# Performance work log

Hardware: AMD Instinct MI355X
Metric: run time of the kernel (lower is better)

The kernel has to match this reference:

```python
import jax, jax.numpy as jnp
import numpy as np
from jax import lax

A = 9            # 3 scales * 3 ratios
H, W = 100, 100  # feature map
STRIDE = 16
PRE_NMS = 6000
POST_NMS = 300
NMS_THRESH = 0.7


def _make_anchors():
    """Standard py-faster-rcnn anchor grid, index order (h, w, a)."""
    base_size = 16.0
    ratios = np.array([0.5, 1.0, 2.0])
    scales = np.array([8.0, 16.0, 32.0])
    x_ctr = y_ctr = (base_size - 1.0) / 2.0
    size = base_size * base_size
    ws_r = np.round(np.sqrt(size / ratios))            # [3]
    hs_r = np.round(ws_r * ratios)                     # [3]
    ws = (ws_r[:, None] * scales[None, :]).reshape(-1)  # [9]
    hs = (hs_r[:, None] * scales[None, :]).reshape(-1)  # [9]
    base = np.stack([x_ctr - 0.5 * (ws - 1), y_ctr - 0.5 * (hs - 1),
                     x_ctr + 0.5 * (ws - 1), y_ctr + 0.5 * (hs - 1)], axis=1)  # [9,4]
    sx, sy = np.meshgrid(np.arange(W) * STRIDE, np.arange(H) * STRIDE)
    shifts = np.stack([sx.ravel(), sy.ravel(), sx.ravel(), sy.ravel()], axis=1)  # [H*W,4]
    anchors = (shifts[:, None, :] + base[None, :, :]).reshape(-1, 4)             # [H*W*A,4]
    return anchors.astype(np.float32)


def setup_inputs() -> dict:
    key = jax.random.key(0)
    k1, k2, k3 = jax.random.split(key, 3)
    return {
        "anchors": jnp.asarray(_make_anchors()),
        "rpn_cls_prob": jax.random.uniform(k1, (1, H, W, 2 * A), dtype=jnp.float32),
        "rpn_bbox_pred": jax.random.normal(k2, (1, H, W, 4 * A), dtype=jnp.float32) * 0.1,
        "rpn_trans_param": jax.random.normal(k3, (1, H, W, 6 * A), dtype=jnp.float32) * 0.1,
        "im_info": jnp.array([H * STRIDE, W * STRIDE, 1.0], dtype=jnp.float32),
    }


def _bbox_transform_inv(anchors, deltas):
    w = anchors[:, 2] - anchors[:, 0] + 1.0
    h = anchors[:, 3] - anchors[:, 1] + 1.0
    cx = anchors[:, 0] + 0.5 * w
    cy = anchors[:, 1] + 0.5 * h
    dx, dy, dw, dh = deltas[:, 0], deltas[:, 1], deltas[:, 2], deltas[:, 3]
    pcx = dx * w + cx
    pcy = dy * h + cy
    pw = jnp.exp(dw) * w
    ph = jnp.exp(dh) * h
    return jnp.stack([pcx - 0.5 * pw, pcy - 0.5 * ph,
                      pcx + 0.5 * pw, pcy + 0.5 * ph], axis=1)


def _clip_boxes(boxes, im_hw):
    im_h, im_w = im_hw[0], im_hw[1]
    x1 = jnp.clip(boxes[:, 0], 0.0, im_w - 1.0)
    y1 = jnp.clip(boxes[:, 1], 0.0, im_h - 1.0)
    x2 = jnp.clip(boxes[:, 2], 0.0, im_w - 1.0)
    y2 = jnp.clip(boxes[:, 3], 0.0, im_h - 1.0)
    return jnp.stack([x1, y1, x2, y2], axis=1)


def _nms_mask(boxes, thresh):
    """Greedy NMS on score-sorted boxes; returns keep mask [N] bool."""
    n = boxes.shape[0]
    x1, y1, x2, y2 = boxes[:, 0], boxes[:, 1], boxes[:, 2], boxes[:, 3]
    areas = (x2 - x1 + 1.0) * (y2 - y1 + 1.0)
    idx = jnp.arange(n)

    def body(i, keep):
        xx1 = jnp.maximum(x1[i], x1)
        yy1 = jnp.maximum(y1[i], y1)
        xx2 = jnp.minimum(x2[i], x2)
        yy2 = jnp.minimum(y2[i], y2)
        iw = jnp.maximum(xx2 - xx1 + 1.0, 0.0)
        ih = jnp.maximum(yy2 - yy1 + 1.0, 0.0)
        inter = iw * ih
        iou = inter / (areas[i] + areas - inter)
        suppress = (iou > thresh) & (idx > i) & keep[i]
        return keep & (~suppress)

    return lax.fori_loop(0, n, body, jnp.ones((n,), dtype=bool))


def _forward(anchors, rpn_cls_prob, rpn_bbox_pred, rpn_trans_param, im_info):
    scores = rpn_cls_prob[:, :, :, A:].reshape(-1)      # fg probs, order (h,w,a)
    deltas = rpn_bbox_pred.reshape(-1, 4)
    trans = rpn_trans_param.reshape(-1, 6)

    proposals = _bbox_transform_inv(anchors, deltas)
    proposals = _clip_boxes(proposals, im_info[:2])

    order = jnp.argsort(-scores)[:PRE_NMS]
    scores = scores[order]
    proposals = proposals[order]
    trans = trans[order]

    keep = _nms_mask(proposals, NMS_THRESH)
    # fixed-size keep indices (score-descending order preserved); padded with 0
    keep_idx = jnp.where(keep, size=POST_NMS, fill_value=0)[0]

    proposals = proposals[keep_idx]
    scores = scores[keep_idx]
    trans = trans[keep_idx]

    batch_inds = jnp.zeros((proposals.shape[0], 1), dtype=proposals.dtype)
    blob = jnp.concatenate([batch_inds, proposals], axis=1)  # [POST_NMS, 5]
    return blob, scores, trans


def reference(anchors, rpn_cls_prob, rpn_bbox_pred, rpn_trans_param, im_info):
    return _forward(anchors, rpn_cls_prob, rpn_bbox_pred, rpn_trans_param, im_info)
```

## Files before the change

kernel.cpp:

```cpp
#include <hip/hip_runtime.h>
#include <stdint.h>
#include <math.h>

#define A_ 9
#define N_ANCH 90000
#define PRE_NMS 6000
#define POST_NMS 300
#define NMS_TH 0.7f
#define NBINS 4096
#define SLOT_CAP 64
#define RANK_BINS 512
#define MASK_W 94
#define NTILE 4465

#define OFF_BCNT   0u
#define OFF_BUCKET 16384u
#define OFF_ORDER  2113536u
#define OFF_TSCORE 2137536u
#define OFF_TBOX   2161536u
#define OFF_MASK   2257536u

typedef unsigned long long u64;
typedef unsigned int u32;

__device__ __forceinline__ int score_bin(float s) {
    int bin = (int)(s * (float)NBINS);
    return bin < 0 ? 0 : (bin > NBINS - 1 ? NBINS - 1 : bin);
}

__global__ void __launch_bounds__(256) k_zero(int4* __restrict__ bcnt4) {
#pragma unroll
    for (int k = 0; k < 4; ++k)
        bcnt4[k * 256 + threadIdx.x] = make_int4(0, 0, 0, 0);
}

__global__ void k_scatter(const float* __restrict__ cls,
                          int* __restrict__ bucketCnt,
                          u64* __restrict__ buckets) {
    int n = blockIdx.x * blockDim.x + threadIdx.x;
    if (n >= N_ANCH) return;
    float s = cls[(n / A_) * (2 * A_) + A_ + (n % A_)];
    int bin = score_bin(s);
    int slot = atomicAdd(&bucketCnt[bin], 1);
    if (slot < SLOT_CAP) {
        u64 key = ((u64)__float_as_uint(s) << 32) | (u64)(0xFFFFFFFFu - (u32)n);
        buckets[(size_t)bin * SLOT_CAP + slot] = key;
    }
}

__device__ __forceinline__ int block_scan(const int* __restrict__ hist,
                                          int* sufs, int* sfx, int* tsh,
                                          int hl[16]) {
    int t = threadIdx.x;
    int csum = 0;
#pragma unroll
    for (int k = 0; k < 16; ++k) { hl[k] = hist[t * 16 + k]; csum += hl[k]; }
    sfx[t] = csum;
    if (t == 0) *tsh = 0;
    __syncthreads();
    for (int off = 1; off < 256; off <<= 1) {
        int v = (t + off < 256) ? sfx[t + off] : 0;
        __syncthreads();
        sfx[t] += v;
        __syncthreads();
    }
    int acc = sfx[t] - csum;
    int best = -1;
#pragma unroll
    for (int k = 15; k >= 0; --k) {
        sufs[t * 16 + k] = acc;
        acc += hl[k];
        if (best < 0 && acc >= PRE_NMS) best = t * 16 + k;
    }
    if (best >= 0) atomicMax(tsh, best);
    __syncthreads();
    return *tsh;
}

__global__ void __launch_bounds__(256) k_rank(const u64* __restrict__ buckets,
                                              const int* __restrict__ bucketCnt,
                                              const float* __restrict__ anchors,
                                              const float* __restrict__ bbox,
                                              const float* __restrict__ im_info,
                                              int* __restrict__ order,
                                              float* __restrict__ tscore,
                                              float* __restrict__ tb) {
#pragma clang fp contract(off)
    __shared__ int sufs[NBINS];
    __shared__ int sfx[256];
    __shared__ int tsh;
    int hl[16];
    int T = block_scan(bucketCnt, sufs, sfx, &tsh, hl);
    int gid = blockIdx.x * 256 + threadIdx.x;
    int bin = (NBINS - RANK_BINS) + (gid >> 6);
    int slot = gid & (SLOT_CAP - 1);
    if (bin < T) return;
    int cnt = bucketCnt[bin];
    if (cnt > SLOT_CAP) cnt = SLOT_CAP;
    if (slot >= cnt) return;
    const u64* bk = buckets + (size_t)bin * SLOT_CAP;
    u64 ki = bk[slot];
    int rank = sufs[bin];
    for (int j = 0; j < cnt; ++j)
        rank += (bk[j] > ki) ? 1 : 0;
    if (rank >= PRE_NMS) return;

    int n = (int)(0xFFFFFFFFu - (u32)(ki & 0xFFFFFFFFull));
    order[rank] = n;
    tscore[rank] = __uint_as_float((u32)(ki >> 32));

    int hw = n / A_, a = n % A_;
    const float* an = anchors + (size_t)n * 4;
    const float* d  = bbox + (size_t)hw * (4 * A_) + a * 4;
    float w  = an[2] - an[0] + 1.0f;
    float h  = an[3] - an[1] + 1.0f;
    float cx = an[0] + 0.5f * w;
    float cy = an[1] + 0.5f * h;
    float pcx = d[0] * w + cx;
    float pcy = d[1] * h + cy;
    float pw  = expf(d[2]) * w;
    float ph  = expf(d[3]) * h;
    float x1 = pcx - 0.5f * pw;
    float y1 = pcy - 0.5f * ph;
    float x2 = pcx + 0.5f * pw;
    float y2 = pcy + 0.5f * ph;
    float im_h = im_info[0], im_w = im_info[1];
    x1 = fminf(fmaxf(x1, 0.0f), im_w - 1.0f);
    y1 = fminf(fmaxf(y1, 0.0f), im_h - 1.0f);
    x2 = fminf(fmaxf(x2, 0.0f), im_w - 1.0f);
    y2 = fminf(fmaxf(y2, 0.0f), im_h - 1.0f);
    tb[rank * 4 + 0] = x1;
    tb[rank * 4 + 1] = y1;
    tb[rank * 4 + 2] = x2;
    tb[rank * 4 + 3] = y2;
}

__global__ void __launch_bounds__(64) k_mask(const float* __restrict__ tb,
                                             u64* __restrict__ mask) {
#pragma clang fp contract(off)
    int u = NTILE - 1 - (int)blockIdx.x;
    int k = (int)((sqrtf(8.0f * (float)u + 1.0f) - 1.0f) * 0.5f);
    while ((k + 1) * (k + 2) / 2 <= u) ++k;
    while (k > 0 && k * (k + 1) / 2 > u) --k;
    int jdx = u - k * (k + 1) / 2;
    int rb = 93 - k, cb = 93 - jdx;

    __shared__ float cbx[64][4];
    __shared__ float car[64];
    int t = threadIdx.x;
    int j0 = cb * 64;
    int jj = j0 + t;
    if (jj < PRE_NMS) {
        float bx1 = tb[jj * 4 + 0], by1 = tb[jj * 4 + 1];
        float bx2 = tb[jj * 4 + 2], by2 = tb[jj * 4 + 3];
        cbx[t][0] = bx1; cbx[t][1] = by1; cbx[t][2] = bx2; cbx[t][3] = by2;
        car[t] = (bx2 - bx1 + 1.0f) * (by2 - by1 + 1.0f);
    } else {
        cbx[t][0] = 0; cbx[t][1] = 0; cbx[t][2] = -2; cbx[t][3] = -2;
        car[t] = 1.0f;
    }
    __syncthreads();
    int row = rb * 64 + t;
    if (row >= PRE_NMS) return;
    float x1 = tb[row * 4 + 0], y1 = tb[row * 4 + 1];
    float x2 = tb[row * 4 + 2], y2 = tb[row * 4 + 3];
    float ai = (x2 - x1 + 1.0f) * (y2 - y1 + 1.0f);
    u64 bits = 0;
    for (int c = 0; c < 64; ++c) {
        int j = j0 + c;
        if (j > row && j < PRE_NMS) {
            float xx1 = fmaxf(x1, cbx[c][0]);
            float yy1 = fmaxf(y1, cbx[c][1]);
            float xx2 = fminf(x2, cbx[c][2]);
            float yy2 = fminf(y2, cbx[c][3]);
            float iw = fmaxf(xx2 - xx1 + 1.0f, 0.0f);
            float ih = fmaxf(yy2 - yy1 + 1.0f, 0.0f);
            float inter = iw * ih;
            float iou = inter / (ai + car[c] - inter);
            if (iou > NMS_TH) bits |= (1ull << c);
        }
    }
    mask[(size_t)row * MASK_W + cb] = bits;
}

__global__ void __launch_bounds__(256) k_reduce_out(const u64* __restrict__ mask,
                                                    const int* __restrict__ order,
                                                    const float* __restrict__ tb,
                                                    const float* __restrict__ tscore,
                                                    const float* __restrict__ trans,
                                                    float* __restrict__ out) {
    __shared__ int keep_s[POST_NMS];
    if (threadIdx.x < 64) {
        const int lane = threadIdx.x;
        int cnt = 0;
        u64 cur = 0;
        u64 dwc = mask[(size_t)lane * MASK_W + 0];
        for (int c = 0; c < MASK_W; ++c) {
            int nc = c + 1;
            u64 dwn = 0;
            if (nc < MASK_W) {
                int rn = nc * 64 + lane;
                if (rn < PRE_NMS) dwn = mask[(size_t)rn * MASK_W + nc];
            }
            int nrows = PRE_NMS - c * 64; if (nrows > 64) nrows = 64;
            u64 vm = (nrows >= 64) ? ~0ull : ((1ull << nrows) - 1ull);
            u32 dlo_v = (u32)dwc, dhi_v = (u32)(dwc >> 32);
            int cnt0 = cnt;
            u64 keptw = 0;
            u64 freeb = (~cur) & vm;
            while (freeb != 0ull && cnt < POST_NMS) {
                u32 bs;
                asm("s_ff1_i32_b64 %0, %1" : "=s"(bs) : "s"(freeb));
                u32 dlo, dhi;
                asm("v_readlane_b32 %0, %1, %2" : "=s"(dlo) : "v"(dlo_v), "s"(bs));
                asm("v_readlane_b32 %0, %1, %2" : "=s"(dhi) : "v"(dhi_v), "s"(bs));
                u64 bit = 1ull << bs;
                keptw |= bit;
                cur |= (((u64)dhi << 32) | (u64)dlo) | bit;
                cnt++;
                freeb = (~cur) & vm;
            }
            if ((keptw >> lane) & 1ull) {
                int pos = cnt0 + __popcll(keptw & ((1ull << lane) - 1ull));
                keep_s[pos] = c * 64 + lane;
            }
            if (cnt >= POST_NMS || nc >= MASK_W) break;
            u64 acc = 0;
#pragma unroll
            for (int s = 0; s < 5; ++s) {
                int p = s * 64 + lane;
                if (p < cnt) {
                    int kr = keep_s[p];
                    acc |= mask[(size_t)kr * MASK_W + nc];
                }
            }
#pragma unroll
            for (int m = 32; m >= 1; m >>= 1)
                acc |= (u64)__shfl_xor((unsigned long long)acc, m, 64);
            u32 clo = __builtin_amdgcn_readfirstlane((u32)acc);
            u32 chi = __builtin_amdgcn_readfirstlane((u32)(acc >> 32));
            cur = ((u64)chi << 32) | (u64)clo;
            dwc = dwn;
        }
        for (int r = cnt + lane; r < POST_NMS; r += 64) keep_s[r] = 0;
    }
    __syncthreads();
    for (int row = threadIdx.x; row < POST_NMS; row += 256) {
        int r = keep_s[row];
        int n = order[r];
        out[row * 5 + 0] = 0.0f;
        out[row * 5 + 1] = tb[r * 4 + 0];
        out[row * 5 + 2] = tb[r * 4 + 1];
        out[row * 5 + 3] = tb[r * 4 + 2];
        out[row * 5 + 4] = tb[r * 4 + 3];
        out[POST_NMS * 5 + row] = tscore[r];
        int hw = n / A_, a = n % A_;
        const float* tp = trans + (size_t)hw * (6 * A_) + a * 6;
#pragma unroll
        for (int c = 0; c < 6; ++c)
            out[POST_NMS * 6 + row * 6 + c] = tp[c];
    }
}

extern "C" void kernel_launch(void* const* d_in, const int* in_sizes, int n_in,
                              void* d_out, int out_size, void* d_ws, size_t ws_size,
                              hipStream_t stream) {
    const float* anchors = (const float*)d_in[0];
    const float* cls     = (const float*)d_in[1];
    const float* bbox    = (const float*)d_in[2];
    const float* trans   = (const float*)d_in[3];
    const float* im_info = (const float*)d_in[4];
    float* out = (float*)d_out;
    char* ws = (char*)d_ws;

    int*   bcnt    = (int*)(ws + OFF_BCNT);
    u64*   buckets = (u64*)(ws + OFF_BUCKET);
    int*   order   = (int*)(ws + OFF_ORDER);
    float* tscore  = (float*)(ws + OFF_TSCORE);
    float* tb      = (float*)(ws + OFF_TBOX);
    u64*   mask    = (u64*)(ws + OFF_MASK);

    int nb = (N_ANCH + 255) / 256;
    k_zero<<<1, 256, 0, stream>>>((int4*)bcnt);
    k_scatter<<<nb, 256, 0, stream>>>(cls, bcnt, buckets);
    k_rank<<<(RANK_BINS * SLOT_CAP) / 256, 256, 0, stream>>>(buckets, bcnt,
                                                             anchors, bbox, im_info,
                                                             order, tscore, tb);
    k_mask<<<NTILE, 64, 0, stream>>>(tb, mask);
    k_reduce_out<<<1, 256, 0, stream>>>(mask, order, tb, tscore, trans, out);
}
```

Measured before the change: 73.92 us.

## Replace full NMS mask kernel with lazy single-block NMS over kept boxes

Drops the precomputed 6000x6000 IoU bitmask kernel and its reduction kernel. In their place is one single-block kernel that stages the top 2048 boxes in LDS, precomputes diagonal 64x64 chunk masks, and for each next chunk tests candidates only against boxes already kept. Because NMS stops once 300 boxes are kept, only a few chunks are likely to be processed, which avoids the O(N^2) mask work and a kernel launch. The cost is serialized per-chunk work on a single CU with two barriers per chunk, and fallback global loads for rows past 2048.

```diff
diff --git a/kernel.cpp b/kernel.cpp
--- a/kernel.cpp
+++ b/kernel.cpp
@@ -11,14 +11,14 @@
 #define SLOT_CAP 64
 #define RANK_BINS 512
 #define MASK_W 94
-#define NTILE 4465
+#define LDSROWS 2048
+#define CPRE 16
 
 #define OFF_BCNT   0u
 #define OFF_BUCKET 16384u
 #define OFF_ORDER  2113536u
 #define OFF_TSCORE 2137536u
 #define OFF_TBOX   2161536u
-#define OFF_MASK   2257536u
 
 typedef unsigned long long u64;
 typedef unsigned int u32;
@@ -135,73 +135,56 @@
     tb[rank * 4 + 3] = y2;
 }
 
-__global__ void __launch_bounds__(64) k_mask(const float* __restrict__ tb,
-                                             u64* __restrict__ mask) {
+__device__ __forceinline__ bool iou_gt(float4 rb, float ra, float4 cb, float ca) {
 #pragma clang fp contract(off)
-    int u = NTILE - 1 - (int)blockIdx.x;
-    int k = (int)((sqrtf(8.0f * (float)u + 1.0f) - 1.0f) * 0.5f);
-    while ((k + 1) * (k + 2) / 2 <= u) ++k;
-    while (k > 0 && k * (k + 1) / 2 > u) --k;
-    int jdx = u - k * (k + 1) / 2;
-    int rb = 93 - k, cb = 93 - jdx;
-
-    __shared__ float cbx[64][4];
-    __shared__ float car[64];
-    int t = threadIdx.x;
-    int j0 = cb * 64;
-    int jj = j0 + t;
-    if (jj < PRE_NMS) {
-        float bx1 = tb[jj * 4 + 0], by1 = tb[jj * 4 + 1];
-        float bx2 = tb[jj * 4 + 2], by2 = tb[jj * 4 + 3];
-        cbx[t][0] = bx1; cbx[t][1] = by1; cbx[t][2] = bx2; cbx[t][3] = by2;
-        car[t] = (bx2 - bx1 + 1.0f) * (by2 - by1 + 1.0f);
-    } else {
-        cbx[t][0] = 0; cbx[t][1] = 0; cbx[t][2] = -2; cbx[t][3] = -2;
-        car[t] = 1.0f;
-    }
-    __syncthreads();
-    int row = rb * 64 + t;
-    if (row >= PRE_NMS) return;
-    float x1 = tb[row * 4 + 0], y1 = tb[row * 4 + 1];
-    float x2 = tb[row * 4 + 2], y2 = tb[row * 4 + 3];
-    float ai = (x2 - x1 + 1.0f) * (y2 - y1 + 1.0f);
-    u64 bits = 0;
-    for (int c = 0; c < 64; ++c) {
-        int j = j0 + c;
-        if (j > row && j < PRE_NMS) {
-            float xx1 = fmaxf(x1, cbx[c][0]);
-            float yy1 = fmaxf(y1, cbx[c][1]);
-            float xx2 = fminf(x2, cbx[c][2]);
-            float yy2 = fminf(y2, cbx[c][3]);
-            float iw = fmaxf(xx2 - xx1 + 1.0f, 0.0f);
-            float ih = fmaxf(yy2 - yy1 + 1.0f, 0.0f);
-            float inter = iw * ih;
-            float iou = inter / (ai + car[c] - inter);
-            if (iou > NMS_TH) bits |= (1ull << c);
-        }
-    }
-    mask[(size_t)row * MASK_W + cb] = bits;
-}
-
-__global__ void __launch_bounds__(256) k_reduce_out(const u64* __restrict__ mask,
-                                                    const int* __restrict__ order,
-                                                    const float* __restrict__ tb,
-                                                    const float* __restrict__ tscore,
-                                                    const float* __restrict__ trans,
-                                                    float* __restrict__ out) {
-    __shared__ int keep_s[POST_NMS];
-    if (threadIdx.x < 64) {
-        const int lane = threadIdx.x;
-        int cnt = 0;
-        u64 cur = 0;
-        u64 dwc = mask[(size_t)lane * MASK_W + 0];
-        for (int c = 0; c < MASK_W; ++c) {
-            int nc = c + 1;
-            u64 dwn = 0;
-            if (nc < MASK_W) {
-                int rn = nc * 64 + lane;
-                if (rn < PRE_NMS) dwn = mask[(size_t)rn * MASK_W + nc];
-            }
+    float xx1 = fmaxf(rb.x, cb.x);
+    float yy1 = fmaxf(rb.y, cb.y);
+    float xx2 = fminf(rb.z, cb.z);
+    float yy2 = fminf(rb.w, cb.w);
+    float iw = fmaxf(xx2 - xx1 + 1.0f, 0.0f);
+    float ih = fmaxf(yy2 - yy1 + 1.0f, 0.0f);
+    float inter = iw * ih;
+    return inter / (ra + ca - inter) > NMS_TH;
+}
+
+__global__ void __launch_bounds__(256)
+k_nms(const float4* __restrict__ tb4, const int* __restrict__ order,
+      const float* __restrict__ tscore, const float* __restrict__ trans,
+      float* __restrict__ out) {
+#pragma clang fp contract(off)
+    __shared__ float4 sbox[LDSROWS];
+    __shared__ float  sarea[LDSROWS];
+    __shared__ u64    sdiag[CPRE][64];
+    __shared__ int    keep_s[POST_NMS];
+    __shared__ u64    curq[4];
+    __shared__ int    ctrl[2];
+    const int t = threadIdx.x;
+    const int lane = t & 63, wq = t >> 6;
+
+    for (int i = t; i < LDSROWS; i += 256) {
+        float4 b = tb4[i];
+        sbox[i] = b;
+        sarea[i] = (b.z - b.x + 1.0f) * (b.w - b.y + 1.0f);
+    }
+    if (t == 0) { ctrl[0] = 0; ctrl[1] = 0; }
+    __syncthreads();
+    for (int g = t; g < CPRE * 64; g += 256) {
+        int ch = g >> 6, row = g & 63;
+        float4 rb = sbox[g]; float ra = sarea[g];
+        u64 bits = 0;
+        for (int c = row + 1; c < 64; ++c) {
+            int j = ch * 64 + c;
+            if (iou_gt(rb, ra, sbox[j], sarea[j])) bits |= 1ull << c;
+        }
+        sdiag[ch][row] = bits;
+    }
+    __syncthreads();
+
+    int cnt = 0;
+    u64 cur = 0;
+    for (int c = 0; c < MASK_W; ++c) {
+        if (wq == 0) {
+            u64 dwc = sdiag[c & (CPRE - 1)][lane];
             int nrows = PRE_NMS - c * 64; if (nrows > 64) nrows = 64;
             u64 vm = (nrows >= 64) ? ~0ull : ((1ull << nrows) - 1ull);
             u32 dlo_v = (u32)dwc, dhi_v = (u32)(dwc >> 32);
@@ -209,8 +192,8 @@
             u64 keptw = 0;
             u64 freeb = (~cur) & vm;
             while (freeb != 0ull && cnt < POST_NMS) {
-                u32 bs;
-                asm("s_ff1_i32_b64 %0, %1" : "=s"(bs) : "s"(freeb));
+                u32 bs = (u32)__builtin_ctzll(freeb);
+                bs = __builtin_amdgcn_readfirstlane(bs);
                 u32 dlo, dhi;
                 asm("v_readlane_b32 %0, %1, %2" : "=s"(dlo) : "v"(dlo_v), "s"(bs));
                 asm("v_readlane_b32 %0, %1, %2" : "=s"(dhi) : "v"(dhi_v), "s"(bs));
@@ -224,41 +207,74 @@
                 int pos = cnt0 + __popcll(keptw & ((1ull << lane) - 1ull));
                 keep_s[pos] = c * 64 + lane;
             }
-            if (cnt >= POST_NMS || nc >= MASK_W) break;
-            u64 acc = 0;
-#pragma unroll
-            for (int s = 0; s < 5; ++s) {
-                int p = s * 64 + lane;
-                if (p < cnt) {
-                    int kr = keep_s[p];
-                    acc |= mask[(size_t)kr * MASK_W + nc];
-                }
-            }
-#pragma unroll
-            for (int m = 32; m >= 1; m >>= 1)
-                acc |= (u64)__shfl_xor((unsigned long long)acc, m, 64);
-            u32 clo = __builtin_amdgcn_readfirstlane((u32)acc);
-            u32 chi = __builtin_amdgcn_readfirstlane((u32)(acc >> 32));
-            cur = ((u64)chi << 32) | (u64)clo;
-            dwc = dwn;
-        }
-        for (int r = cnt + lane; r < POST_NMS; r += 64) keep_s[r] = 0;
-    }
-    __syncthreads();
-    for (int row = threadIdx.x; row < POST_NMS; row += 256) {
+            if (t == 0) {
+                ctrl[0] = cnt;
+                ctrl[1] = (cnt >= POST_NMS || c + 1 >= MASK_W) ? 1 : 0;
+            }
+        }
+        __syncthreads();
+        cnt = ctrl[0];
+        if (ctrl[1]) break;
+        int nc = c + 1;
+        {
+            int jg = nc * 64 + lane;
+            float4 bj; float aj;
+            if (jg < LDSROWS) { bj = sbox[jg]; aj = sarea[jg]; }
+            else if (jg < PRE_NMS) { bj = tb4[jg]; aj = (bj.z - bj.x + 1.0f) * (bj.w - bj.y + 1.0f); }
+            else { bj = make_float4(0.0f, 0.0f, -2.0f, -2.0f); aj = 1.0f; }
+            bool sup = false;
+            for (int k = wq; k < cnt; k += 4) {
+                int r = keep_s[k];
+                float4 br; float ar2;
+                if (r < LDSROWS) { br = sbox[r]; ar2 = sarea[r]; }
+                else { br = tb4[r]; ar2 = (br.z - br.x + 1.0f) * (br.w - br.y + 1.0f); }
+                sup = sup || iou_gt(br, ar2, bj, aj);
+            }
+            u64 bw = __ballot((int)sup);
+            if (lane == 0) curq[wq] = bw;
+        }
+        if (nc >= CPRE && t < 64) {
+            int rg = nc * 64 + t;
+            float4 rb; float ra;
+            if (rg < LDSROWS) { rb = sbox[rg]; ra = sarea[rg]; }
+            else if (rg < PRE_NMS) { rb = tb4[rg]; ra = (rb.z - rb.x + 1.0f) * (rb.w - rb.y + 1.0f); }
+            else { rb = make_float4(0.0f, 0.0f, -2.0f, -2.0f); ra = 1.0f; }
+            u64 bits = 0;
+            for (int cc = t + 1; cc < 64; ++cc) {
+                int j = nc * 64 + cc;
+                float4 cb2; float ca2;
+                if (j < LDSROWS) { cb2 = sbox[j]; ca2 = sarea[j]; }
+                else if (j < PRE_NMS) { cb2 = tb4[j]; ca2 = (cb2.z - cb2.x + 1.0f) * (cb2.w - cb2.y + 1.0f); }
+                else { cb2 = make_float4(0.0f, 0.0f, -2.0f, -2.0f); ca2 = 1.0f; }
+                if (iou_gt(rb, ra, cb2, ca2)) bits |= 1ull << cc;
+            }
+            sdiag[nc & (CPRE - 1)][t] = bits;
+        }
+        __syncthreads();
+        if (wq == 0) {
+            u64 acc = curq[0] | curq[1] | curq[2] | curq[3];
+            u32 lo = __builtin_amdgcn_readfirstlane((u32)acc);
+            u32 hi = __builtin_amdgcn_readfirstlane((u32)(acc >> 32));
+            cur = ((u64)hi << 32) | (u64)lo;
+        }
+    }
+    for (int r = cnt + t; r < POST_NMS; r += 256) keep_s[r] = 0;
+    __syncthreads();
+    const float* tbf = (const float*)tb4;
+    for (int row = t; row < POST_NMS; row += 256) {
         int r = keep_s[row];
         int n = order[r];
         out[row * 5 + 0] = 0.0f;
-        out[row * 5 + 1] = tb[r * 4 + 0];
-        out[row * 5 + 2] = tb[r * 4 + 1];
-        out[row * 5 + 3] = tb[r * 4 + 2];
-        out[row * 5 + 4] = tb[r * 4 + 3];
+        out[row * 5 + 1] = tbf[r * 4 + 0];
+        out[row * 5 + 2] = tbf[r * 4 + 1];
+        out[row * 5 + 3] = tbf[r * 4 + 2];
+        out[row * 5 + 4] = tbf[r * 4 + 3];
         out[POST_NMS * 5 + row] = tscore[r];
         int hw = n / A_, a = n % A_;
         const float* tp = trans + (size_t)hw * (6 * A_) + a * 6;
 #pragma unroll
-        for (int c = 0; c < 6; ++c)
-            out[POST_NMS * 6 + row * 6 + c] = tp[c];
+        for (int cc = 0; cc < 6; ++cc)
+            out[POST_NMS * 6 + row * 6 + cc] = tp[cc];
     }
 }
 
@@ -278,7 +294,6 @@
     int*   order   = (int*)(ws + OFF_ORDER);
     float* tscore  = (float*)(ws + OFF_TSCORE);
     float* tb      = (float*)(ws + OFF_TBOX);
-    u64*   mask    = (u64*)(ws + OFF_MASK);
 
     int nb = (N_ANCH + 255) / 256;
     k_zero<<<1, 256, 0, stream>>>((int4*)bcnt);
@@ -286,6 +301,5 @@
     k_rank<<<(RANK_BINS * SLOT_CAP) / 256, 256, 0, stream>>>(buckets, bcnt,
                                                              anchors, bbox, im_info,
                                                              order, tscore, tb);
-    k_mask<<<NTILE, 64, 0, stream>>>(tb, mask);
-    k_reduce_out<<<1, 256, 0, stream>>>(mask, order, tb, tscore, trans, out);
-}
+    k_nms<<<1, 256, 0, stream>>>((const float4*)tb, order, tscore, trans, out);
+}
```

After: 121.8 us. 64.8% more time.

## Compute NMS mask only for first 1024 boxes, fall back to on-the-fly IoU

Applied to the files above, without the earlier changes.

The IoU bitmask is now built only over the top 16 column blocks (the first 1024 sorted boxes), which cuts the mask kernel from 4465 tiles to 136. The reduction kernel first runs greedy NMS on this partial mask. If fewer than 300 boxes survive, it continues block by block and computes suppression against the kept boxes directly with all 256 threads, plus an intra-block diagonal mask. This avoids building most of the full 6000x6000 mask when 300 boxes are kept early, but adds a slow serial fallback path when many boxes are suppressed.

```diff
diff --git a/kernel.cpp b/kernel.cpp
--- a/kernel.cpp
+++ b/kernel.cpp
@@ -11,7 +11,9 @@
 #define SLOT_CAP 64
 #define RANK_BINS 512
 #define MASK_W 94
-#define NTILE 4465
+#define CAPC 16
+#define MW2 16
+#define NTILE2 136
 
 #define OFF_BCNT   0u
 #define OFF_BUCKET 16384u
@@ -135,40 +137,46 @@
     tb[rank * 4 + 3] = y2;
 }
 
+__device__ __forceinline__ bool iou_gt(float4 rb, float ra, float4 cb, float ca) {
+#pragma clang fp contract(off)
+    float xx1 = fmaxf(rb.x, cb.x);
+    float yy1 = fmaxf(rb.y, cb.y);
+    float xx2 = fminf(rb.z, cb.z);
+    float yy2 = fminf(rb.w, cb.w);
+    float iw = fmaxf(xx2 - xx1 + 1.0f, 0.0f);
+    float ih = fmaxf(yy2 - yy1 + 1.0f, 0.0f);
+    float inter = iw * ih;
+    return inter / (ra + ca - inter) > NMS_TH;
+}
+
 __global__ void __launch_bounds__(64) k_mask(const float* __restrict__ tb,
                                              u64* __restrict__ mask) {
 #pragma clang fp contract(off)
-    int u = NTILE - 1 - (int)blockIdx.x;
-    int k = (int)((sqrtf(8.0f * (float)u + 1.0f) - 1.0f) * 0.5f);
-    while ((k + 1) * (k + 2) / 2 <= u) ++k;
-    while (k > 0 && k * (k + 1) / 2 > u) --k;
-    int jdx = u - k * (k + 1) / 2;
-    int rb = 93 - k, cb = 93 - jdx;
+    int t5 = (int)blockIdx.x;
+    int cb = 0;
+    while ((cb + 1) * (cb + 2) / 2 <= t5) ++cb;
+    int rb = t5 - cb * (cb + 1) / 2;
 
     __shared__ float cbx[64][4];
     __shared__ float car[64];
     int t = threadIdx.x;
     int j0 = cb * 64;
     int jj = j0 + t;
-    if (jj < PRE_NMS) {
+    {
         float bx1 = tb[jj * 4 + 0], by1 = tb[jj * 4 + 1];
         float bx2 = tb[jj * 4 + 2], by2 = tb[jj * 4 + 3];
         cbx[t][0] = bx1; cbx[t][1] = by1; cbx[t][2] = bx2; cbx[t][3] = by2;
         car[t] = (bx2 - bx1 + 1.0f) * (by2 - by1 + 1.0f);
-    } else {
-        cbx[t][0] = 0; cbx[t][1] = 0; cbx[t][2] = -2; cbx[t][3] = -2;
-        car[t] = 1.0f;
     }
     __syncthreads();
     int row = rb * 64 + t;
-    if (row >= PRE_NMS) return;
     float x1 = tb[row * 4 + 0], y1 = tb[row * 4 + 1];
     float x2 = tb[row * 4 + 2], y2 = tb[row * 4 + 3];
     float ai = (x2 - x1 + 1.0f) * (y2 - y1 + 1.0f);
     u64 bits = 0;
     for (int c = 0; c < 64; ++c) {
         int j = j0 + c;
-        if (j > row && j < PRE_NMS) {
+        if (j > row) {
             float xx1 = fmaxf(x1, cbx[c][0]);
             float yy1 = fmaxf(y1, cbx[c][1]);
             float xx2 = fminf(x2, cbx[c][2]);
@@ -180,34 +188,34 @@
             if (iou > NMS_TH) bits |= (1ull << c);
         }
     }
-    mask[(size_t)row * MASK_W + cb] = bits;
-}
-
-__global__ void __launch_bounds__(256) k_reduce_out(const u64* __restrict__ mask,
-                                                    const int* __restrict__ order,
-                                                    const float* __restrict__ tb,
-                                                    const float* __restrict__ tscore,
-                                                    const float* __restrict__ trans,
-                                                    float* __restrict__ out) {
+    mask[(size_t)row * MW2 + cb] = bits;
+}
+
+__global__ void __launch_bounds__(256)
+k_reduce_out(const u64* __restrict__ mask, const float4* __restrict__ tb4,
+             const int* __restrict__ order, const float* __restrict__ tscore,
+             const float* __restrict__ trans, float* __restrict__ out) {
+#pragma clang fp contract(off)
     __shared__ int keep_s[POST_NMS];
-    if (threadIdx.x < 64) {
-        const int lane = threadIdx.x;
+    __shared__ int ctrl[2];
+    __shared__ u64 curq[4];
+    __shared__ u64 sdg[64];
+    const int t = threadIdx.x;
+    const int lane = t & 63, wq = t >> 6;
+
+    if (t < 64) {
         int cnt = 0;
         u64 cur = 0;
-        u64 dwc = mask[(size_t)lane * MASK_W + 0];
-        for (int c = 0; c < MASK_W; ++c) {
+        u64 dwc = mask[(size_t)lane * MW2 + 0];
+        int done = 0;
+        for (int c = 0; c < CAPC; ++c) {
             int nc = c + 1;
             u64 dwn = 0;
-            if (nc < MASK_W) {
-                int rn = nc * 64 + lane;
-                if (rn < PRE_NMS) dwn = mask[(size_t)rn * MASK_W + nc];
-            }
-            int nrows = PRE_NMS - c * 64; if (nrows > 64) nrows = 64;
-            u64 vm = (nrows >= 64) ? ~0ull : ((1ull << nrows) - 1ull);
+            if (nc < CAPC) dwn = mask[(size_t)(nc * 64 + lane) * MW2 + nc];
             u32 dlo_v = (u32)dwc, dhi_v = (u32)(dwc >> 32);
             int cnt0 = cnt;
             u64 keptw = 0;
-            u64 freeb = (~cur) & vm;
+            u64 freeb = ~cur;
             while (freeb != 0ull && cnt < POST_NMS) {
                 u32 bs;
                 asm("s_ff1_i32_b64 %0, %1" : "=s"(bs) : "s"(freeb));
@@ -218,21 +226,19 @@
                 keptw |= bit;
                 cur |= (((u64)dhi << 32) | (u64)dlo) | bit;
                 cnt++;
-                freeb = (~cur) & vm;
+                freeb = ~cur;
             }
             if ((keptw >> lane) & 1ull) {
                 int pos = cnt0 + __popcll(keptw & ((1ull << lane) - 1ull));
                 keep_s[pos] = c * 64 + lane;
             }
-            if (cnt >= POST_NMS || nc >= MASK_W) break;
+            if (cnt >= POST_NMS) { done = 1; break; }
+            if (nc >= CAPC) break;
             u64 acc = 0;
 #pragma unroll
             for (int s = 0; s < 5; ++s) {
                 int p = s * 64 + lane;
-                if (p < cnt) {
-                    int kr = keep_s[p];
-                    acc |= mask[(size_t)kr * MASK_W + nc];
-                }
+                if (p < cnt) acc |= mask[(size_t)keep_s[p] * MW2 + nc];
             }
 #pragma unroll
             for (int m = 32; m >= 1; m >>= 1)
@@ -242,23 +248,94 @@
             cur = ((u64)chi << 32) | (u64)clo;
             dwc = dwn;
         }
-        for (int r = cnt + lane; r < POST_NMS; r += 64) keep_s[r] = 0;
-    }
-    __syncthreads();
-    for (int row = threadIdx.x; row < POST_NMS; row += 256) {
+        if (lane == 0) { ctrl[0] = cnt; ctrl[1] = done; }
+    }
+    __syncthreads();
+
+    int cnt = ctrl[0];
+    if (!ctrl[1]) {
+        for (int c = CAPC; c < MASK_W && cnt < POST_NMS; ++c) {
+            int jg = c * 64 + lane;
+            bool jvalid = jg < PRE_NMS;
+            float4 bj = make_float4(0.0f, 0.0f, -2.0f, -2.0f);
+            float aj = 1.0f;
+            if (jvalid) { bj = tb4[jg]; aj = (bj.z - bj.x + 1.0f) * (bj.w - bj.y + 1.0f); }
+            bool sup = false;
+            for (int k = wq; k < cnt; k += 4) {
+                int r = keep_s[k];
+                float4 br = tb4[r];
+                float ar2 = (br.z - br.x + 1.0f) * (br.w - br.y + 1.0f);
+                if (jvalid) sup = sup || iou_gt(br, ar2, bj, aj);
+            }
+            u64 bw = __ballot((int)sup);
+            if (lane == 0) curq[wq] = bw;
+            if (t < 64) {
+                u64 bits = 0;
+                if (jvalid) {
+                    for (int cc = t + 1; cc < 64; ++cc) {
+                        int j2 = c * 64 + cc;
+                        if (j2 < PRE_NMS) {
+                            float4 cb2 = tb4[j2];
+                            float ca2 = (cb2.z - cb2.x + 1.0f) * (cb2.w - cb2.y + 1.0f);
+                            if (iou_gt(bj, aj, cb2, ca2)) bits |= 1ull << cc;
+                        }
+                    }
+                }
+                sdg[t] = bits;
+            }
+            __syncthreads();
+            if (t < 64) {
+                u64 cur = curq[0] | curq[1] | curq[2] | curq[3];
+                u64 dwc = sdg[lane];
+                int nrows = PRE_NMS - c * 64; if (nrows > 64) nrows = 64;
+                u64 vm = (nrows >= 64) ? ~0ull : ((1ull << nrows) - 1ull);
+                u32 dlo_v = (u32)dwc, dhi_v = (u32)(dwc >> 32);
+                int cnt0 = cnt;
+                u64 keptw = 0;
+                u64 freeb = (~cur) & vm;
+                while (freeb != 0ull && cnt < POST_NMS) {
+                    u32 bs = __builtin_amdgcn_readfirstlane((u32)__builtin_ctzll(freeb));
+                    u32 dlo, dhi;
+                    asm("v_readlane_b32 %0, %1, %2" : "=s"(dlo) : "v"(dlo_v), "s"(bs));
+                    asm("v_readlane_b32 %0, %1, %2" : "=s"(dhi) : "v"(dhi_v), "s"(bs));
+                    u64 bit = 1ull << bs;
+                    keptw |= bit;
+                    cur |= (((u64)dhi << 32) | (u64)dlo) | bit;
+                    cnt++;
+                    freeb = (~cur) & vm;
+                }
+                if ((keptw >> lane) & 1ull) {
+                    int pos = cnt0 + __popcll(keptw & ((1ull << lane) - 1ull));
+                    keep_s[pos] = c * 64 + lane;
+                }
+                if (lane == 0) {
+                    ctrl[0] = cnt;
+                    ctrl[1] = (cnt >= POST_NMS) ? 1 : 0;
+                }
+            }
+            __syncthreads();
+            cnt = ctrl[0];
+            if (ctrl[1]) break;
+        }
+    }
+
+    for (int r = cnt + t; r < POST_NMS; r += 256) keep_s[r] = 0;
+    __syncthreads();
+    const float* tbf = (const float*)tb4;
+    for (int row = t; row < POST_NMS; row += 256) {
         int r = keep_s[row];
         int n = order[r];
         out[row * 5 + 0] = 0.0f;
-        out[row * 5 + 1] = tb[r * 4 + 0];
-        out[row * 5 + 2] = tb[r * 4 + 1];
-        out[row * 5 + 3] = tb[r * 4 + 2];
-        out[row * 5 + 4] = tb[r * 4 + 3];
+        out[row * 5 + 1] = tbf[r * 4 + 0];
+        out[row * 5 + 2] = tbf[r * 4 + 1];
+        out[row * 5 + 3] = tbf[r * 4 + 2];
+        out[row * 5 + 4] = tbf[r * 4 + 3];
         out[POST_NMS * 5 + row] = tscore[r];
         int hw = n / A_, a = n % A_;
         const float* tp = trans + (size_t)hw * (6 * A_) + a * 6;
 #pragma unroll
-        for (int c = 0; c < 6; ++c)
-            out[POST_NMS * 6 + row * 6 + c] = tp[c];
+        for (int cc = 0; cc < 6; ++cc)
+            out[POST_NMS * 6 + row * 6 + cc] = tp[cc];
     }
 }
 
@@ -286,6 +363,7 @@
     k_rank<<<(RANK_BINS * SLOT_CAP) / 256, 256, 0, stream>>>(buckets, bcnt,
                                                              anchors, bbox, im_info,
                                                              order, tscore, tb);
-    k_mask<<<NTILE, 64, 0, stream>>>(tb, mask);
-    k_reduce_out<<<1, 256, 0, stream>>>(mask, order, tb, tscore, trans, out);
-}
+    k_mask<<<NTILE2, 64, 0, stream>>>(tb, mask);
+    k_reduce_out<<<1, 256, 0, stream>>>(mask, (const float4*)tb,
+                                        order, tscore, trans, out);
+}
```

Result: faster. 60.37 us (median of 2 runs) (-18.3%).
